# Performance work log

Measured on AMD Instinct MI355X. Metric: run time of the kernel, lower is better.

Reference implementation:

```python
import jax, jax.numpy as jnp
import numpy as np

B, T, V = 4, 2048, 2048
D = 256   # state_dim
R = 512   # inner_dim
EPS = float(jnp.finfo(jnp.float32).eps)  # F.rms_norm default eps = dtype eps


def rms_norm(x):
    return x * jax.lax.rsqrt(jnp.mean(x * x, axis=-1, keepdims=True) + EPS)


def setup_inputs() -> dict:
    key = jax.random.key(0)
    ks = jax.random.split(key, 9)
    std = 0.02
    return {
        "x": jax.random.normal(ks[0], (B, T, V), dtype=jnp.float32),
        "Wq": jax.random.normal(ks[1], (D, V), dtype=jnp.float32) * std,
        "Wk": jax.random.normal(ks[2], (D, V), dtype=jnp.float32) * std,
        "Wv": jax.random.normal(ks[3], (D, V), dtype=jnp.float32) * std,
        "Wo": jax.random.normal(ks[4], (V, D), dtype=jnp.float32) * std,
        "decay_logit": jnp.float32(3.0),
        "q_out_scale": jnp.float32(0.1),
        "Wdown": jax.random.normal(ks[5], (R, V), dtype=jnp.float32) * std,
        "Wup": jax.random.normal(ks[6], (V, R), dtype=jnp.float32) * std,
        "t_bias": jnp.zeros((R,), dtype=jnp.float32),
        "t_out_scale": jnp.float32(0.1),
        "q_scale": jnp.ones((1,), dtype=jnp.float32),
        "t_scale": jnp.ones((1,), dtype=jnp.float32),
    }


def qtable(x, Wq, Wk, Wv, Wo, decay_logit, out_scale):
    # x: (B,T,V)
    q = jnp.einsum('btv,dv->btd', x, Wq)
    k = jnp.einsum('btv,dv->btd', x, Wk)
    v = jnp.einsum('btv,dv->btd', x, Wv)
    scores = jnp.einsum('btd,bsd->bts', q, k)  # (B,T,T)
    decay = jax.nn.sigmoid(decay_logit)
    pos = jnp.arange(T)
    diff = pos[None, :] - pos[:, None]  # diff[t,s] = s - t ... matches torch (unsqueeze(0)-unsqueeze(1))
    causal = (diff > 0).astype(jnp.float32)
    weights = decay ** jnp.clip(diff.astype(jnp.float32) - 1.0, 0.0, None) * causal
    scores = scores * weights[None, :, :]
    retrieved = jnp.einsum('bts,bsd->btd', scores, v)
    return jnp.einsum('btd,vd->btv', retrieved, Wo) * out_scale


def transform(x, Wdown, Wup, bias, out_scale):
    h = jnp.einsum('btv,rv->btr', x, Wdown) + bias
    h = jax.nn.gelu(h, approximate=False)
    return jnp.einsum('btr,vr->btv', h, Wup) * out_scale


def reference(x, Wq, Wk, Wv, Wo, decay_logit, q_out_scale,
              Wdown, Wup, t_bias, t_out_scale, q_scale, t_scale):
    x = x + q_scale * qtable(rms_norm(x), Wq, Wk, Wv, Wo, decay_logit, q_out_scale)
    x = x + t_scale * transform(rms_norm(x), Wdown, Wup, t_bias, t_out_scale)
    return x
```

## Files before the change

### kernel.cpp

```cpp
#include <hip/hip_runtime.h>
#include <cmath>

typedef _Float16 f16;
typedef _Float16 f16x8 __attribute__((ext_vector_type(8)));
typedef _Float16 f16x4 __attribute__((ext_vector_type(4)));
typedef float f32x4 __attribute__((ext_vector_type(4)));

#define MFMA16(a, b, c) __builtin_amdgcn_mfma_f32_16x16x32_f16(a, b, c, 0, 0, 0)

static constexpr int Bsz = 4;
static constexpr int T = 2048;
static constexpr int V = 2048;
static constexpr int D = 256;
static constexpr int R = 512;
static constexpr int M = Bsz * T;

__device__ __forceinline__ void load_lds16(const f16* g, f16* l) {
    __builtin_amdgcn_global_load_lds(
        (const __attribute__((address_space(1))) unsigned int*)(unsigned long long)g,
        (__attribute__((address_space(3))) unsigned int*)(unsigned int)(unsigned long long)l,
        16, 0, 0);
}

__global__ __launch_bounds__(256) void conv_all(const float* __restrict__ s0,
                                                const float* __restrict__ s1,
                                                const float* __restrict__ s2,
                                                const float* __restrict__ s3,
                                                const float* __restrict__ s4,
                                                const float* __restrict__ s5,
                                                f16* __restrict__ dst) {
    int idx = (blockIdx.x * 256 + threadIdx.x) * 4;
    if (idx >= 4194304) return;
    const float* src; int off;
    if      (idx <  524288) { src = s0; off = idx; }
    else if (idx < 1048576) { src = s1; off = idx - 524288; }
    else if (idx < 1572864) { src = s2; off = idx - 1048576; }
    else if (idx < 2097152) { src = s3; off = idx - 1572864; }
    else if (idx < 3145728) { src = s4; off = idx - 2097152; }
    else                    { src = s5; off = idx - 3145728; }
    float4 v = *(const float4*)&src[off];
    f16x4 o;
    o[0] = (f16)v.x; o[1] = (f16)v.y; o[2] = (f16)v.z; o[3] = (f16)v.w;
    *(f16x4*)&dst[idx] = o;
}

__global__ __launch_bounds__(256) void rmsnorm_kernel(const float* __restrict__ x,
                                                      f16* __restrict__ out) {
    int row = blockIdx.x;
    const float* xr = x + (size_t)row * V;
    int tid = threadIdx.x;
    float4 v0 = ((const float4*)xr)[tid];
    float4 v1 = ((const float4*)xr)[tid + 256];
    float ss = v0.x * v0.x + v0.y * v0.y + v0.z * v0.z + v0.w * v0.w
             + v1.x * v1.x + v1.y * v1.y + v1.z * v1.z + v1.w * v1.w;
    #pragma unroll
    for (int o = 32; o > 0; o >>= 1) ss += __shfl_xor(ss, o);
    __shared__ float wsum[4];
    if ((tid & 63) == 0) wsum[tid >> 6] = ss;
    __syncthreads();
    float tot = wsum[0] + wsum[1] + wsum[2] + wsum[3];
    float s = rsqrtf(tot / (float)V + 1.1920929e-07f);
    f16* orow = out + (size_t)row * V;
    f16x4 o0, o1;
    o0[0] = (f16)(v0.x * s); o0[1] = (f16)(v0.y * s);
    o0[2] = (f16)(v0.z * s); o0[3] = (f16)(v0.w * s);
    o1[0] = (f16)(v1.x * s); o1[1] = (f16)(v1.y * s);
    o1[2] = (f16)(v1.z * s); o1[3] = (f16)(v1.w * s);
    *(f16x4*)&orow[tid * 4] = o0;
    *(f16x4*)&orow[1024 + tid * 4] = o1;
}

struct GemmEpi {
    const float* residf;
    const f16* residh;
    float* outf;
    f16* outh;
    f16* out_q; f16* out_k; f16* out_vT;
    f16* out_h;
    const float* bias;
    const float* sA; const float* sB;
    float* rowss;
};

template <int MODE>
__device__ __forceinline__ void epi_store(const GemmEpi& e, float s, f32x4 a,
                                          int gm_base, int gn) {
    #pragma unroll
    for (int i = 0; i < 4; i++) {
        int gm = gm_base + i;
        float vv = a[i];
        if (MODE == 0) {
            if (gn < 256) {
                e.out_q[(size_t)gm * D + gn] = (f16)vv;
            } else if (gn < 512) {
                e.out_k[(size_t)gm * D + (gn - 256)] = (f16)vv;
            } else {
                int d = gn - 512;
                int b = gm >> 11, t = gm & 2047;
                e.out_vT[((size_t)b * D + d) * T + t] = (f16)vv;
            }
        } else if (MODE == 1) {
            size_t o = (size_t)gm * V + gn;
            e.outh[o] = (f16)(e.residf[o] + s * vv);
        } else if (MODE == 2) {
            float sc = rsqrtf(e.rowss[gm] * (1.f / 2048.f) + 1.1920929e-07f);
            float z = sc * vv + e.bias[gn];
            float g = 0.5f * z * (1.f + erff(z * 0.70710678118654752f));
            e.out_h[(size_t)gm * R + gn] = (f16)g;
        } else {
            size_t o = (size_t)gm * V + gn;
            e.outf[o] = (float)e.residh[o] + s * vv;
        }
    }
}

template <int MODE>
__global__ __launch_bounds__(256) void gemm_nt(const f16* __restrict__ A,
                                               const f16* __restrict__ Bm,
                                               int K, GemmEpi e) {
    __shared__ f16 Asl[2][128 * 32];
    __shared__ f16 Bsl[2][128 * 32];
    int tid = threadIdx.x;
    int lane = tid & 63, wv = tid >> 6;
    int wm = wv >> 1, wn = wv & 1;
    int quad = lane >> 4, l16 = lane & 15;
    int m0 = blockIdx.x * 128, n0 = blockIdx.y * 128;
    f32x4 acc[4][4] = {};

    int srow = lane >> 2;
    int scg = (lane & 3) ^ ((lane >> 3) & 3);
    const f16* Ag0 = &A[(size_t)(m0 + 16 * wv + srow) * K + scg * 8];
    const f16* Ag1 = &A[(size_t)(m0 + 16 * (wv + 4) + srow) * K + scg * 8];
    const f16* Bg0 = &Bm[(size_t)(n0 + 16 * wv + srow) * K + scg * 8];
    const f16* Bg1 = &Bm[(size_t)(n0 + 16 * (wv + 4) + srow) * K + scg * 8];
    int lo0 = (16 * wv) * 32, lo1 = (16 * (wv + 4)) * 32;

    int fs = quad ^ ((l16 >> 1) & 3);
    int niter = K >> 5;

    load_lds16(Ag0, &Asl[0][lo0]);
    load_lds16(Ag1, &Asl[0][lo1]);
    load_lds16(Bg0, &Bsl[0][lo0]);
    load_lds16(Bg1, &Bsl[0][lo1]);

    for (int i = 0; i < niter; i++) {
        int cur = i & 1;
        __builtin_amdgcn_s_barrier();
        if (i + 1 < niter) {
            int k0 = (i + 1) << 5;
            int nb = cur ^ 1;
            load_lds16(Ag0 + k0, &Asl[nb][lo0]);
            load_lds16(Ag1 + k0, &Asl[nb][lo1]);
            load_lds16(Bg0 + k0, &Bsl[nb][lo0]);
            load_lds16(Bg1 + k0, &Bsl[nb][lo1]);
            asm volatile("s_waitcnt vmcnt(4)" ::: "memory");
        } else {
            asm volatile("s_waitcnt vmcnt(0)" ::: "memory");
        }
        __builtin_amdgcn_s_barrier();
        f16x8 af[4], bf[4];
        #pragma unroll
        for (int j = 0; j < 4; j++)
            af[j] = *(const f16x8*)&Asl[cur][(64 * wm + 16 * j + l16) * 32 + fs * 8];
        #pragma unroll
        for (int j = 0; j < 4; j++)
            bf[j] = *(const f16x8*)&Bsl[cur][(64 * wn + 16 * j + l16) * 32 + fs * 8];
        #pragma unroll
        for (int mi = 0; mi < 4; mi++)
            #pragma unroll
            for (int ni = 0; ni < 4; ni++)
                acc[mi][ni] = MFMA16(af[mi], bf[ni], acc[mi][ni]);
    }

    float s = 0.f;
    if (MODE == 1 || MODE == 3) s = e.sA[0] * e.sB[0];

    if constexpr (MODE == 1) {
        float* rbuf = (float*)&Asl[0][0];
        __syncthreads();
        #pragma unroll
        for (int mi = 0; mi < 4; mi++) {
            #pragma unroll
            for (int i = 0; i < 4; i++) {
                int rl = 64 * wm + 16 * mi + quad * 4 + i;
                int gm = m0 + rl;
                float p = 0.f;
                #pragma unroll
                for (int ni = 0; ni < 4; ni++) {
                    int gn = n0 + 64 * wn + 16 * ni + l16;
                    size_t o = (size_t)gm * V + gn;
                    float val = e.residf[o] + s * acc[mi][ni][i];
                    e.outh[o] = (f16)val;
                    p += val * val;
                }
                rbuf[rl * 32 + wn * 16 + l16] = p;
            }
        }
        __syncthreads();
        if (tid < 128) {
            float tot = 0.f;
            #pragma unroll
            for (int j = 0; j < 32; j++) tot += rbuf[tid * 32 + j];
            atomicAdd(&e.rowss[m0 + tid], tot);
        }
    } else {
        #pragma unroll
        for (int mi = 0; mi < 4; mi++)
            #pragma unroll
            for (int ni = 0; ni < 4; ni++)
                epi_store<MODE>(e, s, acc[mi][ni],
                                m0 + 64 * wm + 16 * mi + quad * 4,
                                n0 + 64 * wn + 16 * ni + l16);
    }
}

template <int MODE>
__global__ __launch_bounds__(256) void gemm_nt_k64(const f16* __restrict__ A,
                                                   const f16* __restrict__ Bm,
                                                   int K, GemmEpi e) {
    __shared__ f16 Asl[2][128 * 64];
    __shared__ f16 Bsl[2][128 * 64];
    int tid = threadIdx.x;
    int lane = tid & 63, wv = tid >> 6;
    int wm = wv >> 1, wn = wv & 1;
    int quad = lane >> 4, l16 = lane & 15;
    int m0 = blockIdx.x * 128, n0 = blockIdx.y * 128;
    f32x4 acc[4][4] = {};

    int r8 = lane >> 3;
    int gcol = (lane & 7) ^ r8;
    const f16* Ag[4]; const f16* Bg[4]; int lo[4];
    #pragma unroll
    for (int j = 0; j < 4; j++) {
        int rbase = 8 * (wv + 4 * j);
        Ag[j] = &A[(size_t)(m0 + rbase + r8) * K + gcol * 8];
        Bg[j] = &Bm[(size_t)(n0 + rbase + r8) * K + gcol * 8];
        lo[j] = rbase * 64;
    }
    int niter = K >> 6;

    #pragma unroll
    for (int j = 0; j < 4; j++) {
        load_lds16(Ag[j], &Asl[0][lo[j]]);
        load_lds16(Bg[j], &Bsl[0][lo[j]]);
    }

    for (int i = 0; i < niter; i++) {
        int cur = i & 1;
        __builtin_amdgcn_s_barrier();
        if (i + 1 < niter) {
            int k0 = (i + 1) << 6;
            int nb = cur ^ 1;
            #pragma unroll
            for (int j = 0; j < 4; j++) {
                load_lds16(Ag[j] + k0, &Asl[nb][lo[j]]);
                load_lds16(Bg[j] + k0, &Bsl[nb][lo[j]]);
            }
            asm volatile("s_waitcnt vmcnt(8)" ::: "memory");
        } else {
            asm volatile("s_waitcnt vmcnt(0)" ::: "memory");
        }
        __builtin_amdgcn_s_barrier();
        #pragma unroll
        for (int kk = 0; kk < 2; kk++) {
            f16x8 af[4], bf[4];
            #pragma unroll
            for (int j = 0; j < 4; j++) {
                int row = 64 * wm + 16 * j + l16;
                int sl = (kk * 4 + quad) ^ (l16 & 7);
                af[j] = *(const f16x8*)&Asl[cur][row * 64 + sl * 8];
            }
            #pragma unroll
            for (int j = 0; j < 4; j++) {
                int row = 64 * wn + 16 * j + l16;
                int sl = (kk * 4 + quad) ^ (l16 & 7);
                bf[j] = *(const f16x8*)&Bsl[cur][row * 64 + sl * 8];
            }
            #pragma unroll
            for (int mi = 0; mi < 4; mi++)
                #pragma unroll
                for (int ni = 0; ni < 4; ni++)
                    acc[mi][ni] = MFMA16(af[mi], bf[ni], acc[mi][ni]);
        }
    }

    float s = 0.f;
    if (MODE == 1 || MODE == 3) s = e.sA[0] * e.sB[0];
    #pragma unroll
    for (int mi = 0; mi < 4; mi++)
        #pragma unroll
        for (int ni = 0; ni < 4; ni++)
            epi_store<MODE>(e, s, acc[mi][ni],
                            m0 + 64 * wm + 16 * mi + quad * 4,
                            n0 + 64 * wn + 16 * ni + l16);
}

__global__ __launch_bounds__(256) void attn_kernel(const f16* __restrict__ q,
                                                   const f16* __restrict__ k,
                                                   const f16* __restrict__ vT,
                                                   f16* __restrict__ ret,
                                                   const float* __restrict__ decay_logit) {
    __shared__ f16 Psl[32 * 72];
    int tid = threadIdx.x, lane = tid & 63, wv = tid >> 6;
    int quad = lane >> 4, l16 = lane & 15;
    int b = blockIdx.y, t0 = blockIdx.x * 32;
    const f16* qb = q + (size_t)b * T * D;
    const f16* kb = k + (size_t)b * T * D;
    const f16* vb = vT + (size_t)b * D * T;
    f16* rb = ret + (size_t)b * T * D;

    float dl = decay_logit[0];
    float decay = 1.f / (1.f + expf(-dl));
    float l2d = log2f(decay);
    float nl2d = -l2d;

    f16x8 qf[2][8];
    #pragma unroll
    for (int mi = 0; mi < 2; mi++)
        #pragma unroll
        for (int kk = 0; kk < 8; kk++)
            qf[mi][kk] = *(const f16x8*)&qb[(size_t)(t0 + 16 * mi + l16) * D + kk * 32 + quad * 8];

    f32x4 acc2[2][4] = {};

    for (int s0 = t0; s0 < T; s0 += 64) {
        if ((float)(s0 - t0 - 32) * nl2d > 25.f) break;
        int srow = s0 + 16 * wv + l16;
        int srcl = srow < T ? srow : T - 1;
        f32x4 sacc[2] = {};
        #pragma unroll
        for (int kk = 0; kk < 8; kk++) {
            f16x8 bf = *(const f16x8*)&kb[(size_t)srcl * D + kk * 32 + quad * 8];
            sacc[0] = MFMA16(qf[0][kk], bf, sacc[0]);
            sacc[1] = MFMA16(qf[1][kk], bf, sacc[1]);
        }
        __syncthreads();
        #pragma unroll
        for (int mi = 0; mi < 2; mi++) {
            #pragma unroll
            for (int i = 0; i < 4; i++) {
                int t_ = t0 + 16 * mi + quad * 4 + i;
                int diff = srow - t_;
                float w = (diff > 0 && srow < T) ? exp2f((float)(diff - 1) * l2d) : 0.f;
                Psl[(16 * mi + quad * 4 + i) * 72 + 16 * wv + l16] = (f16)(sacc[mi][i] * w);
            }
        }
        __syncthreads();
        #pragma unroll
        for (int kk = 0; kk < 2; kk++) {
            int sb = s0 + kk * 32 + quad * 8;
            if (sb >= T) sb = T - 8;
            f16x8 pa[2], vf[4];
            #pragma unroll
            for (int mi = 0; mi < 2; mi++)
                pa[mi] = *(const f16x8*)&Psl[(16 * mi + l16) * 72 + kk * 32 + quad * 8];
            #pragma unroll
            for (int ni = 0; ni < 4; ni++)
                vf[ni] = *(const f16x8*)&vb[(size_t)(64 * wv + 16 * ni + l16) * T + sb];
            #pragma unroll
            for (int mi = 0; mi < 2; mi++)
                #pragma unroll
                for (int ni = 0; ni < 4; ni++)
                    acc2[mi][ni] = MFMA16(pa[mi], vf[ni], acc2[mi][ni]);
        }
    }

    #pragma unroll
    for (int mi = 0; mi < 2; mi++) {
        #pragma unroll
        for (int ni = 0; ni < 4; ni++) {
            int t_ = t0 + 16 * mi + quad * 4;
            int d_ = 64 * wv + 16 * ni + l16;
            #pragma unroll
            for (int i = 0; i < 4; i++)
                rb[(size_t)(t_ + i) * D + d_] = (f16)acc2[mi][ni][i];
        }
    }
}

extern "C" void kernel_launch(void* const* d_in, const int* in_sizes, int n_in,
                              void* d_out, int out_size, void* d_ws, size_t ws_size,
                              hipStream_t stream) {
    const float* x           = (const float*)d_in[0];
    const float* Wq          = (const float*)d_in[1];
    const float* Wk          = (const float*)d_in[2];
    const float* Wv          = (const float*)d_in[3];
    const float* Wo          = (const float*)d_in[4];
    const float* decay_logit = (const float*)d_in[5];
    const float* q_out_scale = (const float*)d_in[6];
    const float* Wdown       = (const float*)d_in[7];
    const float* Wup         = (const float*)d_in[8];
    const float* t_bias      = (const float*)d_in[9];
    const float* t_out_scale = (const float*)d_in[10];
    const float* q_scale     = (const float*)d_in[11];
    const float* t_scale     = (const float*)d_in[12];

    char* ws = (char*)d_ws;
    f16* Wqkv16  = (f16*)ws;  ws += (size_t)768 * V * 2;
    f16* Wo16    = (f16*)ws;  ws += (size_t)V * D * 2;
    f16* Wdown16 = (f16*)ws;  ws += (size_t)R * V * 2;
    f16* Wup16   = (f16*)ws;  ws += (size_t)V * R * 2;
    f16* xn16    = (f16*)ws;  ws += (size_t)M * V * 2;
    f16* q16     = (f16*)ws;  ws += (size_t)M * D * 2;
    f16* k16     = (f16*)ws;  ws += (size_t)M * D * 2;
    f16* vT16    = (f16*)ws;  ws += (size_t)Bsz * D * T * 2;
    f16* ret16   = (f16*)ws;  ws += (size_t)M * D * 2;
    f16* x2_16   = (f16*)ws;  ws += (size_t)M * V * 2;
    float* rowss = (float*)ws; ws += (size_t)M * 4;
    f16* h16     = q16;

    float* out = (float*)d_out;

    conv_all<<<dim3(4096), 256, 0, stream>>>(Wq, Wk, Wv, Wo, Wdown, Wup, Wqkv16);
    hipMemsetAsync(rowss, 0, (size_t)M * 4, stream);

    rmsnorm_kernel<<<dim3(M), 256, 0, stream>>>(x, xn16);

    {
        GemmEpi e = {};
        e.out_q = q16; e.out_k = k16; e.out_vT = vT16;
        gemm_nt_k64<0><<<dim3(M / 128, 768 / 128), 256, 0, stream>>>(xn16, Wqkv16, V, e);
    }

    attn_kernel<<<dim3(T / 32, Bsz), 256, 0, stream>>>(q16, k16, vT16, ret16, decay_logit);

    {
        GemmEpi e = {};
        e.residf = x; e.outh = x2_16; e.sA = q_scale; e.sB = q_out_scale;
        e.rowss = rowss;
        gemm_nt<1><<<dim3(M / 128, V / 128), 256, 0, stream>>>(ret16, Wo16, D, e);
    }


    {
        GemmEpi e = {};
        e.out_h = h16; e.bias = t_bias; e.rowss = rowss;
        gemm_nt_k64<2><<<dim3(M / 128, R / 128), 256, 0, stream>>>(x2_16, Wdown16, V, e);
    }

    {
        GemmEpi e = {};
        e.residh = x2_16; e.outf = out; e.sA = t_scale; e.sB = t_out_scale;
        gemm_nt<3><<<dim3(M / 128, V / 128), 256, 0, stream>>>(h16, Wup16, R, e);
    }
}
```

Baseline: 306.1 us.

## Fuse weight conversion, rmsnorm and rowss reset; use 128x192 tiles for QKV GEMM

Result: no change. 303.6 us (-0.8%).

```diff
diff --git a/kernel.cpp b/kernel.cpp
--- a/kernel.cpp
+++ b/kernel.cpp
@@ -22,33 +22,35 @@
         16, 0, 0);
 }
 
-__global__ __launch_bounds__(256) void conv_all(const float* __restrict__ s0,
-                                                const float* __restrict__ s1,
-                                                const float* __restrict__ s2,
-                                                const float* __restrict__ s3,
-                                                const float* __restrict__ s4,
-                                                const float* __restrict__ s5,
-                                                f16* __restrict__ dst) {
-    int idx = (blockIdx.x * 256 + threadIdx.x) * 4;
-    if (idx >= 4194304) return;
-    const float* src; int off;
-    if      (idx <  524288) { src = s0; off = idx; }
-    else if (idx < 1048576) { src = s1; off = idx - 524288; }
-    else if (idx < 1572864) { src = s2; off = idx - 1048576; }
-    else if (idx < 2097152) { src = s3; off = idx - 1572864; }
-    else if (idx < 3145728) { src = s4; off = idx - 2097152; }
-    else                    { src = s5; off = idx - 3145728; }
-    float4 v = *(const float4*)&src[off];
-    f16x4 o;
-    o[0] = (f16)v.x; o[1] = (f16)v.y; o[2] = (f16)v.z; o[3] = (f16)v.w;
-    *(f16x4*)&dst[idx] = o;
-}
-
-__global__ __launch_bounds__(256) void rmsnorm_kernel(const float* __restrict__ x,
-                                                      f16* __restrict__ out) {
-    int row = blockIdx.x;
+__global__ __launch_bounds__(256) void prep_kernel(const float* __restrict__ s0,
+                                                   const float* __restrict__ s1,
+                                                   const float* __restrict__ s2,
+                                                   const float* __restrict__ s3,
+                                                   const float* __restrict__ s4,
+                                                   const float* __restrict__ s5,
+                                                   f16* __restrict__ dst,
+                                                   const float* __restrict__ x,
+                                                   f16* __restrict__ xn,
+                                                   float* __restrict__ rowss) {
+    int bid = blockIdx.x;
+    int tid = threadIdx.x;
+    if (bid < 4096) {
+        int idx = (bid * 256 + tid) * 4;
+        const float* src; int off;
+        if      (idx <  524288) { src = s0; off = idx; }
+        else if (idx < 1048576) { src = s1; off = idx - 524288; }
+        else if (idx < 1572864) { src = s2; off = idx - 1048576; }
+        else if (idx < 2097152) { src = s3; off = idx - 1572864; }
+        else if (idx < 3145728) { src = s4; off = idx - 2097152; }
+        else                    { src = s5; off = idx - 3145728; }
+        float4 v = *(const float4*)&src[off];
+        f16x4 o;
+        o[0] = (f16)v.x; o[1] = (f16)v.y; o[2] = (f16)v.z; o[3] = (f16)v.w;
+        *(f16x4*)&dst[idx] = o;
+        return;
+    }
+    int row = bid - 4096;
     const float* xr = x + (size_t)row * V;
-    int tid = threadIdx.x;
     float4 v0 = ((const float4*)xr)[tid];
     float4 v1 = ((const float4*)xr)[tid + 256];
     float ss = v0.x * v0.x + v0.y * v0.y + v0.z * v0.z + v0.w * v0.w
@@ -60,7 +62,7 @@
     __syncthreads();
     float tot = wsum[0] + wsum[1] + wsum[2] + wsum[3];
     float s = rsqrtf(tot / (float)V + 1.1920929e-07f);
-    f16* orow = out + (size_t)row * V;
+    f16* orow = xn + (size_t)row * V;
     f16x4 o0, o1;
     o0[0] = (f16)(v0.x * s); o0[1] = (f16)(v0.y * s);
     o0[2] = (f16)(v0.z * s); o0[3] = (f16)(v0.w * s);
@@ -68,6 +70,7 @@
     o1[2] = (f16)(v1.z * s); o1[3] = (f16)(v1.w * s);
     *(f16x4*)&orow[tid * 4] = o0;
     *(f16x4*)&orow[1024 + tid * 4] = o1;
+    if (tid == 0) rowss[row] = 0.f;
 }
 
 struct GemmEpi {
@@ -115,6 +118,78 @@
 }
 
 template <int MODE>
+__global__ __launch_bounds__(256) void gemm_nt_192(const f16* __restrict__ A,
+                                                   const f16* __restrict__ Bm,
+                                                   int K, GemmEpi e) {
+    __shared__ f16 Asl[2][128 * 32];
+    __shared__ f16 Bsl[2][192 * 32];
+    int tid = threadIdx.x;
+    int lane = tid & 63, wv = tid >> 6;
+    int wm = wv >> 1, wn = wv & 1;
+    int quad = lane >> 4, l16 = lane & 15;
+    int m0 = blockIdx.x * 128, n0 = blockIdx.y * 192;
+    f32x4 acc[4][6] = {};
+
+    int srow = lane >> 2;
+    int scg = (lane & 3) ^ ((lane >> 3) & 3);
+    const f16* Ag0 = &A[(size_t)(m0 + 16 * wv + srow) * K + scg * 8];
+    const f16* Ag1 = &A[(size_t)(m0 + 16 * (wv + 4) + srow) * K + scg * 8];
+    const f16* Bg0 = &Bm[(size_t)(n0 + 16 * wv + srow) * K + scg * 8];
+    const f16* Bg1 = &Bm[(size_t)(n0 + 16 * (wv + 4) + srow) * K + scg * 8];
+    const f16* Bg2 = &Bm[(size_t)(n0 + 16 * (wv + 8) + srow) * K + scg * 8];
+    int lo0 = (16 * wv) * 32, lo1 = (16 * (wv + 4)) * 32, lo2 = (16 * (wv + 8)) * 32;
+
+    int fs = quad ^ ((l16 >> 1) & 3);
+    int niter = K >> 5;
+
+    load_lds16(Ag0, &Asl[0][lo0]);
+    load_lds16(Ag1, &Asl[0][lo1]);
+    load_lds16(Bg0, &Bsl[0][lo0]);
+    load_lds16(Bg1, &Bsl[0][lo1]);
+    load_lds16(Bg2, &Bsl[0][lo2]);
+
+    for (int i = 0; i < niter; i++) {
+        int cur = i & 1;
+        __builtin_amdgcn_s_barrier();
+        if (i + 1 < niter) {
+            int k0 = (i + 1) << 5;
+            int nb = cur ^ 1;
+            load_lds16(Ag0 + k0, &Asl[nb][lo0]);
+            load_lds16(Ag1 + k0, &Asl[nb][lo1]);
+            load_lds16(Bg0 + k0, &Bsl[nb][lo0]);
+            load_lds16(Bg1 + k0, &Bsl[nb][lo1]);
+            load_lds16(Bg2 + k0, &Bsl[nb][lo2]);
+            asm volatile("s_waitcnt vmcnt(5)" ::: "memory");
+        } else {
+            asm volatile("s_waitcnt vmcnt(0)" ::: "memory");
+        }
+        __builtin_amdgcn_s_barrier();
+        f16x8 af[4], bf[6];
+        #pragma unroll
+        for (int j = 0; j < 4; j++)
+            af[j] = *(const f16x8*)&Asl[cur][(64 * wm + 16 * j + l16) * 32 + fs * 8];
+        #pragma unroll
+        for (int j = 0; j < 6; j++)
+            bf[j] = *(const f16x8*)&Bsl[cur][(96 * wn + 16 * j + l16) * 32 + fs * 8];
+        #pragma unroll
+        for (int mi = 0; mi < 4; mi++)
+            #pragma unroll
+            for (int ni = 0; ni < 6; ni++)
+                acc[mi][ni] = MFMA16(af[mi], bf[ni], acc[mi][ni]);
+    }
+
+    float s = 0.f;
+    if (MODE == 1 || MODE == 3) s = e.sA[0] * e.sB[0];
+    #pragma unroll
+    for (int mi = 0; mi < 4; mi++)
+        #pragma unroll
+        for (int ni = 0; ni < 6; ni++)
+            epi_store<MODE>(e, s, acc[mi][ni],
+                            m0 + 64 * wm + 16 * mi + quad * 4,
+                            n0 + 96 * wn + 16 * ni + l16);
+}
+
+template <int MODE>
 __global__ __launch_bounds__(256) void gemm_nt(const f16* __restrict__ A,
                                                const f16* __restrict__ Bm,
                                                int K, GemmEpi e) {
@@ -411,15 +486,13 @@
 
     float* out = (float*)d_out;
 
-    conv_all<<<dim3(4096), 256, 0, stream>>>(Wq, Wk, Wv, Wo, Wdown, Wup, Wqkv16);
-    hipMemsetAsync(rowss, 0, (size_t)M * 4, stream);
-
-    rmsnorm_kernel<<<dim3(M), 256, 0, stream>>>(x, xn16);
+    prep_kernel<<<dim3(12288), 256, 0, stream>>>(Wq, Wk, Wv, Wo, Wdown, Wup,
+                                                 Wqkv16, x, xn16, rowss);
 
     {
         GemmEpi e = {};
         e.out_q = q16; e.out_k = k16; e.out_vT = vT16;
-        gemm_nt_k64<0><<<dim3(M / 128, 768 / 128), 256, 0, stream>>>(xn16, Wqkv16, V, e);
+        gemm_nt_192<0><<<dim3(M / 128, 768 / 192), 256, 0, stream>>>(xn16, Wqkv16, V, e);
     }
 
     attn_kernel<<<dim3(T / 32, Bsz), 256, 0, stream>>>(q16, k16, vT16, ret16, decay_logit);
@@ -431,7 +504,6 @@
         gemm_nt<1><<<dim3(M / 128, V / 128), 256, 0, stream>>>(ret16, Wo16, D, e);
     }
 
-
     {
         GemmEpi e = {};
         e.out_h = h16; e.bias = t_bias; e.rowss = rowss;
```
